# Kernel tuning notes

Measured on AMD Instinct MI355X. Metric: run time of the kernel, lower is better.

Reference implementation:

```python
import jax, jax.numpy as jnp
import numpy as np

# Device / physics constants for group_idx = 0 (from the original source)
V_REF = 0.25
G_MIN = 1.0 / 983.3
G_MAX = 1.0 / 281.3
N_AVG = 2.132
N_STD = 0.095

BATCH, N_IN, N_OUT = 256, 784, 512


def setup_inputs() -> dict:
    key = jax.random.key(0)
    k1, k2, k3, k4, k5, k6 = jax.random.split(key, 6)
    stdv = 1.0 / np.sqrt(N_IN)
    x = jax.random.normal(k1, (BATCH, N_IN), dtype=jnp.float32)
    # weights initialized N(0.5, stdv) as in build()
    w_pos = 0.5 + stdv * jax.random.normal(k2, (N_IN, N_OUT), dtype=jnp.float32)
    w_neg = 0.5 + stdv * jax.random.normal(k3, (N_IN, N_OUT), dtype=jnp.float32)
    b_pos = 0.5 * jnp.ones((N_OUT,), dtype=jnp.float32)
    b_neg = 0.5 * jnp.ones((N_OUT,), dtype=jnp.float32)
    # per-device IV nonlinearity samples n ~ N(n_avg, n_std), shape = G shape
    n_param = N_AVG + N_STD * jax.random.normal(k6, (N_IN + 1, 2 * N_OUT), dtype=jnp.float32)
    return {"x": x, "w_pos": w_pos, "w_neg": w_neg, "b_pos": b_pos,
            "b_neg": b_neg, "n_param": n_param}


def _memristor_dense(x, w_pos, w_neg, b_pos, b_neg, n_param):
    # Fold biases in as an extra crossbar row, interleave pos/neg columns.
    cw_pos = jnp.concatenate([w_pos, b_pos[None, :]], axis=0)   # (n_in+1, n_out)
    cw_neg = jnp.concatenate([w_neg, b_neg[None, :]], axis=0)
    weights = jnp.stack([cw_pos, cw_neg], axis=-1)              # (n_in+1, n_out, 2)
    weights = weights.reshape(cw_pos.shape[0], -1)              # (n_in+1, 2*n_out) interleaved
    inputs = jnp.concatenate(
        [x, jnp.ones((x.shape[0], 1), dtype=x.dtype)], axis=1)  # (batch, n_in+1)

    max_weight = jnp.max(jnp.abs(weights))
    k_G = (G_MAX - G_MIN) / max_weight
    # weight params -> conductances (params are nonnegative by construction)
    G = G_MIN + k_G * jnp.clip(weights, 0.0, None)              # (n_in+1, 2*n_out)

    k_V = 2.0 * V_REF
    V = k_V * inputs                                            # (batch, n_in+1)

    # Nonlinear IV: I = sign(V) * V_ref * G * (|V|/V_ref)^log2(n)
    exponent = jnp.log2(n_param)                                # (n_in+1, 2*n_out)
    ratio = jnp.abs(V) / V_REF                                  # (batch, n_in+1)
    I_ind = (jnp.sign(V)[:, :, None] * V_REF * G[None, :, :]
             * ratio[:, :, None] ** exponent[None, :, :])       # (batch, n_in+1, 2*n_out)
    I = jnp.sum(I_ind, axis=1)                                  # (batch, 2*n_out)

    # Currents -> outputs: differential pairs, undo V and G scaling
    I_total = I[:, 0::2] - I[:, 1::2]                           # (batch, n_out)
    y = I_total / (k_V * k_G)
    return y


def reference(x, w_pos, w_neg, b_pos, b_neg, n_param):
    return _memristor_dense(x, w_pos, w_neg, b_pos, b_neg, n_param)
```

## Files before the change

kernel.cpp:

```cpp
#include <hip/hip_runtime.h>

#define NIN   784
#define NOUT  512
#define NROWS 785
#define BATCH 256
#define CHUNK 16
#define NZ    50

static constexpr float G_MIN_F  = (float)(1.0 / 983.3);
static constexpr float G_DIFF_F = (float)(1.0 / 281.3 - 1.0 / 983.3);

__device__ __forceinline__ float dlog2(float v) { return __builtin_amdgcn_logf(v); }
__device__ __forceinline__ float dexp2(float v) { return __builtin_amdgcn_exp2f(v); }

__device__ __forceinline__ float load_maxw(const float* __restrict__ pm, int tid) {
    float m = pm[tid & 127];
    #pragma unroll
    for (int off = 1; off < 64; off <<= 1)
        m = fmaxf(m, __shfl_xor(m, off, 64));
    __shared__ float sm2[4];
    if ((tid & 63) == 0) sm2[tid >> 6] = m;
    __syncthreads();
    return fmaxf(fmaxf(sm2[0], sm2[1]), fmaxf(sm2[2], sm2[3]));
}

__global__ __launch_bounds__(256) void mk_max(
    const float* __restrict__ wp, const float* __restrict__ wn,
    const float* __restrict__ bp, const float* __restrict__ bn,
    float* __restrict__ part, float4* __restrict__ out4)
{
    const int gid = blockIdx.x * 256 + threadIdx.x;
    out4[gid] = make_float4(0.f, 0.f, 0.f, 0.f);

    float m = 0.0f;
    const int n4 = NIN * NOUT / 4;
    const float4* wp4 = (const float4*)wp;
    const float4* wn4 = (const float4*)wn;
    for (int idx = gid; idx < n4; idx += gridDim.x * 256) {
        float4 a = wp4[idx], b = wn4[idx];
        m = fmaxf(m, fmaxf(fmaxf(fabsf(a.x), fabsf(a.y)), fmaxf(fabsf(a.z), fabsf(a.w))));
        m = fmaxf(m, fmaxf(fmaxf(fabsf(b.x), fabsf(b.y)), fmaxf(fabsf(b.z), fabsf(b.w))));
    }
    if (blockIdx.x == 0 && threadIdx.x < NOUT) {
        m = fmaxf(m, fabsf(bp[threadIdx.x]));
        m = fmaxf(m, fabsf(bn[threadIdx.x]));
    }
    #pragma unroll
    for (int off = 1; off < 64; off <<= 1)
        m = fmaxf(m, __shfl_xor(m, off, 64));
    __shared__ float sm[4];
    if ((threadIdx.x & 63) == 0) sm[threadIdx.x >> 6] = m;
    __syncthreads();
    if (threadIdx.x == 0)
        part[blockIdx.x] = fmaxf(fmaxf(sm[0], sm[1]), fmaxf(sm[2], sm[3]));
}

__global__ __launch_bounds__(256) void mk_main(
    const float* __restrict__ x,  const float* __restrict__ wp,
    const float* __restrict__ wn, const float* __restrict__ bp,
    const float* __restrict__ bn, const float* __restrict__ npar,
    const float* __restrict__ pm, float* __restrict__ out)
{
    const int tid = threadIdx.x;
    const float maxw = load_maxw(pm, tid);
    const float kG = G_DIFF_F / maxw;
    const float C  = 0.5f * maxw / G_DIFF_F;

    const int tx = tid & 63;
    const int ty = tid >> 6;
    const int j0 = blockIdx.x * 64;
    const int jp = j0 + tx;
    const int b0 = blockIdx.y * 32;
    const int i0 = blockIdx.z * CHUNK;

    __shared__ float4 Tb[CHUNK * 64];
    __shared__ float2 Ls[CHUNK][33];

    #pragma unroll
    for (int k = 0; k < 4; ++k) {
        const int p  = tid + k * 256;
        const int ii = p >> 6, jj = p & 63;
        const int i  = i0 + ii;
        float4 r = make_float4(0.f, 0.f, 0.f, 0.f);
        if (i < NROWS) {
            const float wpv = (i < NIN) ? wp[i * NOUT + j0 + jj] : bp[j0 + jj];
            const float wnv = (i < NIN) ? wn[i * NOUT + j0 + jj] : bn[j0 + jj];
            const float2 nv = *(const float2*)(&npar[i * (2 * NOUT) + 2 * (j0 + jj)]);
            r.x = dlog2(nv.x);
            r.y = dlog2(fmaf(kG, fmaxf(wpv, 0.0f), G_MIN_F));
            r.z = dlog2(nv.y);
            r.w = dlog2(fmaf(kG, fmaxf(wnv, 0.0f), G_MIN_F));
        }
        Tb[p] = r;
    }

    #pragma unroll
    for (int k = 0; k < 2; ++k) {
        const int t  = tid + k * 256;
        const int bb = t >> 4, ii = t & 15;
        const int i  = i0 + ii;
        float L = 0.0f, s = 0.0f;
        if (i < NIN) {
            const float v = x[(b0 + bb) * NIN + i];
            s = (v > 0.0f) ? 1.0f : ((v < 0.0f) ? -1.0f : 0.0f);
            L = dlog2(2.0f * fabsf(v));
        } else if (i == NIN) { L = 1.0f; s = 1.0f; }
        Ls[ii][bb] = make_float2(L, s);
    }
    __syncthreads();

    float acc[8];
    #pragma unroll
    for (int b = 0; b < 8; ++b) acc[b] = 0.0f;

    #pragma unroll
    for (int ii = 0; ii < CHUNK; ++ii) {
        const float4 tv = Tb[ii * 64 + tx];
        #pragma unroll
        for (int b = 0; b < 8; ++b) {
            const float2 ls = Ls[ii][ty * 8 + b];
            const float tp = dexp2(fmaf(tv.x, ls.x, tv.y));
            const float tn = dexp2(fmaf(tv.z, ls.x, tv.w));
            acc[b] = fmaf(ls.y, tp - tn, acc[b]);
        }
    }

    #pragma unroll
    for (int b = 0; b < 8; ++b)
        unsafeAtomicAdd(&out[(b0 + ty * 8 + b) * NOUT + jp], C * acc[b]);
}

extern "C" void kernel_launch(void* const* d_in, const int* in_sizes, int n_in,
                              void* d_out, int out_size, void* d_ws, size_t ws_size,
                              hipStream_t stream) {
    const float* x    = (const float*)d_in[0];
    const float* wp   = (const float*)d_in[1];
    const float* wn   = (const float*)d_in[2];
    const float* bp   = (const float*)d_in[3];
    const float* bn   = (const float*)d_in[4];
    const float* npar = (const float*)d_in[5];
    float*        out = (float*)d_out;
    float*         pm = (float*)d_ws;

    mk_max<<<128, 256, 0, stream>>>(wp, wn, bp, bn, pm, (float4*)out);

    dim3 grid(NOUT / 64, BATCH / 32, NZ);
    mk_main<<<grid, 256, 0, stream>>>(x, wp, wn, bp, bn, npar, pm, out);
}
```

Baseline: 38.40 us.

## Precompute input log/sign table in a separate kernel and read it via scalar loads

Adds a kernel that computes log2(2|x|) and sign for every input row and batch into a padded workspace table. The main kernel drops its per-block shared-memory staging of these values and instead reads them straight from global memory with wave-uniform addresses (readfirstlane), which should let them become scalar loads. This removes redundant log computations repeated across the output-column blocks and shrinks shared-memory traffic. The cost is an extra launch and the workspace write and read.

```diff
diff --git a/kernel.cpp b/kernel.cpp
--- a/kernel.cpp
+++ b/kernel.cpp
@@ -3,6 +3,7 @@
 #define NIN   784
 #define NOUT  512
 #define NROWS 785
+#define NPAD  800
 #define BATCH 256
 #define CHUNK 16
 #define NZ    50
@@ -12,6 +13,10 @@
 
 __device__ __forceinline__ float dlog2(float v) { return __builtin_amdgcn_logf(v); }
 __device__ __forceinline__ float dexp2(float v) { return __builtin_amdgcn_exp2f(v); }
+
+#define WS_PM_OFF 0
+#define WS_LX_OFF 4096
+#define WS_TOTAL  (WS_LX_OFF + (size_t)NPAD * BATCH * 8)
 
 __device__ __forceinline__ float load_maxw(const float* __restrict__ pm, int tid) {
     float m = pm[tid & 127];
@@ -55,11 +60,25 @@
         part[blockIdx.x] = fmaxf(fmaxf(sm[0], sm[1]), fmaxf(sm[2], sm[3]));
 }
 
+__global__ __launch_bounds__(256) void mk_lx(
+    const float* __restrict__ x, float2* __restrict__ lx)
+{
+    const int t  = blockIdx.x * 256 + threadIdx.x;
+    const int i  = t >> 8, bb = t & 255;
+    float L = 0.0f, s = 0.0f;
+    if (i < NIN) {
+        const float v = x[bb * NIN + i];
+        s = (v > 0.0f) ? 1.0f : ((v < 0.0f) ? -1.0f : 0.0f);
+        L = dlog2(2.0f * fabsf(v));
+    } else if (i == NIN) { L = 1.0f; s = 1.0f; }
+    lx[i * BATCH + bb] = make_float2(L, s);
+}
+
 __global__ __launch_bounds__(256) void mk_main(
-    const float* __restrict__ x,  const float* __restrict__ wp,
-    const float* __restrict__ wn, const float* __restrict__ bp,
-    const float* __restrict__ bn, const float* __restrict__ npar,
-    const float* __restrict__ pm, float* __restrict__ out)
+    const float* __restrict__ wp, const float* __restrict__ wn,
+    const float* __restrict__ bp, const float* __restrict__ bn,
+    const float* __restrict__ npar, const float* __restrict__ pm,
+    const float2* __restrict__ lx, float* __restrict__ out)
 {
     const int tid = threadIdx.x;
     const float maxw = load_maxw(pm, tid);
@@ -68,13 +87,13 @@
 
     const int tx = tid & 63;
     const int ty = tid >> 6;
+    const int tyu = __builtin_amdgcn_readfirstlane(ty);
     const int j0 = blockIdx.x * 64;
     const int jp = j0 + tx;
     const int b0 = blockIdx.y * 32;
     const int i0 = blockIdx.z * CHUNK;
 
     __shared__ float4 Tb[CHUNK * 64];
-    __shared__ float2 Ls[CHUNK][33];
 
     #pragma unroll
     for (int k = 0; k < 4; ++k) {
@@ -93,35 +112,26 @@
         }
         Tb[p] = r;
     }
-
-    #pragma unroll
-    for (int k = 0; k < 2; ++k) {
-        const int t  = tid + k * 256;
-        const int bb = t >> 4, ii = t & 15;
-        const int i  = i0 + ii;
-        float L = 0.0f, s = 0.0f;
-        if (i < NIN) {
-            const float v = x[(b0 + bb) * NIN + i];
-            s = (v > 0.0f) ? 1.0f : ((v < 0.0f) ? -1.0f : 0.0f);
-            L = dlog2(2.0f * fabsf(v));
-        } else if (i == NIN) { L = 1.0f; s = 1.0f; }
-        Ls[ii][bb] = make_float2(L, s);
-    }
     __syncthreads();
 
     float acc[8];
     #pragma unroll
     for (int b = 0; b < 8; ++b) acc[b] = 0.0f;
 
+    const float2* lsrow = &lx[i0 * BATCH + b0 + tyu * 8];
+
     #pragma unroll
     for (int ii = 0; ii < CHUNK; ++ii) {
         const float4 tv = Tb[ii * 64 + tx];
+        float2 lsv[8];
+        #pragma unroll
+        for (int b = 0; b < 8; ++b)
+            lsv[b] = lsrow[ii * BATCH + b];
         #pragma unroll
         for (int b = 0; b < 8; ++b) {
-            const float2 ls = Ls[ii][ty * 8 + b];
-            const float tp = dexp2(fmaf(tv.x, ls.x, tv.y));
-            const float tn = dexp2(fmaf(tv.z, ls.x, tv.w));
-            acc[b] = fmaf(ls.y, tp - tn, acc[b]);
+            const float tp = dexp2(fmaf(tv.x, lsv[b].x, tv.y));
+            const float tn = dexp2(fmaf(tv.z, lsv[b].x, tv.w));
+            acc[b] = fmaf(lsv[b].y, tp - tn, acc[b]);
         }
     }
 
@@ -140,10 +150,12 @@
     const float* bn   = (const float*)d_in[4];
     const float* npar = (const float*)d_in[5];
     float*        out = (float*)d_out;
-    float*         pm = (float*)d_ws;
+    float*         pm = (float*)((char*)d_ws + WS_PM_OFF);
+    float2*        lx = (float2*)((char*)d_ws + WS_LX_OFF);
 
     mk_max<<<128, 256, 0, stream>>>(wp, wn, bp, bn, pm, (float4*)out);
+    mk_lx<<<NPAD * BATCH / 256, 256, 0, stream>>>(x, lx);
 
     dim3 grid(NOUT / 64, BATCH / 32, NZ);
-    mk_main<<<grid, 256, 0, stream>>>(x, wp, wn, bp, bn, npar, pm, out);
+    mk_main<<<grid, 256, 0, stream>>>(wp, wn, bp, bn, npar, pm, lx, out);
 }
```

Result: slower. 43.85 us (+14.2%).

## Process two row chunks per block and broadcast inputs via readlane

Applied to the files above, without the earlier changes.

Each block now processes two 16-row chunks of the reduction dimension, which halves the z-grid and the number of atomic adds to the output. The per-batch log-input and sign values move from a shared-memory table into registers and are broadcast with wave readlane (scalar) operations instead of LDS reads. This cuts atomic traffic and LDS loads in the inner loop. In exchange it adds an extra barrier, serialises the per-chunk table build with the compute inside each block, and halves the number of blocks.

```diff
diff --git a/kernel.cpp b/kernel.cpp
--- a/kernel.cpp
+++ b/kernel.cpp
@@ -5,13 +5,17 @@
 #define NROWS 785
 #define BATCH 256
 #define CHUNK 16
-#define NZ    50
+#define NZB   25
 
 static constexpr float G_MIN_F  = (float)(1.0 / 983.3);
 static constexpr float G_DIFF_F = (float)(1.0 / 281.3 - 1.0 / 983.3);
 
 __device__ __forceinline__ float dlog2(float v) { return __builtin_amdgcn_logf(v); }
 __device__ __forceinline__ float dexp2(float v) { return __builtin_amdgcn_exp2f(v); }
+
+__device__ __forceinline__ float rdlane(float v, int lane) {
+    return __int_as_float(__builtin_amdgcn_readlane(__float_as_int(v), lane));
+}
 
 __device__ __forceinline__ float load_maxw(const float* __restrict__ pm, int tid) {
     float m = pm[tid & 127];
@@ -71,57 +75,65 @@
     const int j0 = blockIdx.x * 64;
     const int jp = j0 + tx;
     const int b0 = blockIdx.y * 32;
-    const int i0 = blockIdx.z * CHUNK;
 
     __shared__ float4 Tb[CHUNK * 64];
-    __shared__ float2 Ls[CHUNK][33];
-
-    #pragma unroll
-    for (int k = 0; k < 4; ++k) {
-        const int p  = tid + k * 256;
-        const int ii = p >> 6, jj = p & 63;
-        const int i  = i0 + ii;
-        float4 r = make_float4(0.f, 0.f, 0.f, 0.f);
-        if (i < NROWS) {
-            const float wpv = (i < NIN) ? wp[i * NOUT + j0 + jj] : bp[j0 + jj];
-            const float wnv = (i < NIN) ? wn[i * NOUT + j0 + jj] : bn[j0 + jj];
-            const float2 nv = *(const float2*)(&npar[i * (2 * NOUT) + 2 * (j0 + jj)]);
-            r.x = dlog2(nv.x);
-            r.y = dlog2(fmaf(kG, fmaxf(wpv, 0.0f), G_MIN_F));
-            r.z = dlog2(nv.y);
-            r.w = dlog2(fmaf(kG, fmaxf(wnv, 0.0f), G_MIN_F));
-        }
-        Tb[p] = r;
-    }
-
-    #pragma unroll
-    for (int k = 0; k < 2; ++k) {
-        const int t  = tid + k * 256;
-        const int bb = t >> 4, ii = t & 15;
-        const int i  = i0 + ii;
-        float L = 0.0f, s = 0.0f;
-        if (i < NIN) {
-            const float v = x[(b0 + bb) * NIN + i];
-            s = (v > 0.0f) ? 1.0f : ((v < 0.0f) ? -1.0f : 0.0f);
-            L = dlog2(2.0f * fabsf(v));
-        } else if (i == NIN) { L = 1.0f; s = 1.0f; }
-        Ls[ii][bb] = make_float2(L, s);
-    }
-    __syncthreads();
 
     float acc[8];
     #pragma unroll
     for (int b = 0; b < 8; ++b) acc[b] = 0.0f;
 
     #pragma unroll
-    for (int ii = 0; ii < CHUNK; ++ii) {
-        const float4 tv = Tb[ii * 64 + tx];
+    for (int c = 0; c < 2; ++c) {
+        const int i0 = (blockIdx.z * 2 + c) * CHUNK;
+        if (c) __syncthreads();
+
         #pragma unroll
-        for (int b = 0; b < 8; ++b) {
-            const float2 ls = Ls[ii][ty * 8 + b];
-            const float tp = dexp2(fmaf(tv.x, ls.x, tv.y));
-            const float tn = dexp2(fmaf(tv.z, ls.x, tv.w));
-            acc[b] = fmaf(ls.y, tp - tn, acc[b]);
+        for (int k = 0; k < 4; ++k) {
+            const int p  = tid + k * 256;
+            const int ii = p >> 6, jj = p & 63;
+            const int i  = i0 + ii;
+            float4 r = make_float4(0.f, 0.f, 0.f, 0.f);
+            if (i < NROWS) {
+                const float wpv = (i < NIN) ? wp[i * NOUT + j0 + jj] : bp[j0 + jj];
+                const float wnv = (i < NIN) ? wn[i * NOUT + j0 + jj] : bn[j0 + jj];
+                const float2 nv = *(const float2*)(&npar[i * (2 * NOUT) + 2 * (j0 + jj)]);
+                r.x = dlog2(nv.x);
+                r.y = dlog2(fmaf(kG, fmaxf(wpv, 0.0f), G_MIN_F));
+                r.z = dlog2(nv.y);
+                r.w = dlog2(fmaf(kG, fmaxf(wnv, 0.0f), G_MIN_F));
+            }
+            Tb[p] = r;
+        }
+
+        float Lv[2], sv[2];
+        #pragma unroll
+        for (int k = 0; k < 2; ++k) {
+            const int ii = tx & 15;
+            const int bb = (tx >> 4) + 4 * k;
+            const int i  = i0 + ii;
+            float L = 0.0f, s = 0.0f;
+            if (i < NIN) {
+                const float v = x[(b0 + ty * 8 + bb) * NIN + i];
+                s = (v > 0.0f) ? 1.0f : ((v < 0.0f) ? -1.0f : 0.0f);
+                L = dlog2(2.0f * fabsf(v));
+            } else if (i == NIN) { L = 1.0f; s = 1.0f; }
+            Lv[k] = L; sv[k] = s;
+        }
+        __syncthreads();
+
+        #pragma unroll
+        for (int ii = 0; ii < CHUNK; ++ii) {
+            const float4 tv = Tb[ii * 64 + tx];
+            #pragma unroll
+            for (int b = 0; b < 8; ++b) {
+                const int ln = (b & 3) * 16 + ii;
+                const int k  = b >> 2;
+                const float Lb = rdlane(Lv[k], ln);
+                const float sb = rdlane(sv[k], ln);
+                const float tp = dexp2(fmaf(tv.x, Lb, tv.y));
+                const float tn = dexp2(fmaf(tv.z, Lb, tv.w));
+                acc[b] = fmaf(sb, tp - tn, acc[b]);
+            }
         }
     }
 
@@ -144,6 +156,6 @@
 
     mk_max<<<128, 256, 0, stream>>>(wp, wn, bp, bn, pm, (float4*)out);
 
-    dim3 grid(NOUT / 64, BATCH / 32, NZ);
+    dim3 grid(NOUT / 64, BATCH / 32, NZB);
     mk_main<<<grid, 256, 0, stream>>>(x, wp, wn, bp, bn, npar, pm, out);
 }
```

Result: slower. 52.50 us (+36.7%).
